# Kernel optimization log

Hardware: AMD Instinct MI355X
Metric: run time of the kernel (lower is better)

Reference implementation:

```python
import jax, jax.numpy as jnp
import numpy as np

LOCAL_RADIUS = 5


def setup_inputs() -> dict:
    key = jax.random.key(0)
    k1, k2, k3 = jax.random.split(key, 3)
    B, K, C, H = 4, 4096, 256, 128
    x = jax.random.normal(k1, (B, K, C), dtype=jnp.float32)
    W1 = jax.random.normal(k2, (C, H), dtype=jnp.float32) * (1.0 / np.sqrt(C))
    b1 = jnp.zeros((H,), dtype=jnp.float32)
    W2 = jax.random.normal(k3, (H, 1), dtype=jnp.float32) * (1.0 / np.sqrt(H))
    b2 = jnp.zeros((1,), dtype=jnp.float32)
    return {"x": x, "W1": W1, "b1": b1, "W2": W2, "b2": b2}


def reference(x, W1, b1, W2, b2):
    # x: [B, k, C]. The MLP score for column j is independent of the row i,
    # so compute it once per token instead of per (i, window) as in the torch loop.
    B, k, C = x.shape
    s = (jnp.tanh(x @ W1 + b1) @ W2 + b2)[..., 0]  # [B, k]
    idx = jnp.arange(k)
    band = (jnp.abs(idx[:, None] - idx[None, :]) <= LOCAL_RADIUS)  # [k, k]
    # Outside the band the original leaves scores at 0.0 (not -inf), so
    # out-of-window positions still contribute exp(0)=1 to the softmax.
    scores = jnp.where(band[None, :, :], s[:, None, :], jnp.float32(0.0))  # [B, k, k]
    weights = jax.nn.softmax(scores, axis=-1)  # [B, k, k]
    weighted = jnp.einsum('bij,bjc->bic', weights, x)  # [B, k, C]
    return weighted, weights
```

## Files before the change

kernel.cpp:

```cpp
#include <hip/hip_runtime.h>
#include <math.h>

#define B_ 4
#define K_ 4096
#define C_ 256
#define H_ 128
#define RAD 5
#define ROWS 8

typedef float floatx4 __attribute__((ext_vector_type(4)));


__global__ __launch_bounds__(128) void score_kernel(
    const float* __restrict__ x, const float* __restrict__ W1,
    const float* __restrict__ b1, const float* __restrict__ W2,
    const float* __restrict__ b2, float* __restrict__ s_out)
{
    const int tid = threadIdx.x;
    const int t0 = blockIdx.x * 8;
    const float* xr[8];
    #pragma unroll
    for (int t = 0; t < 8; ++t) xr[t] = x + (size_t)(t0 + t) * C_;

    float acc[8];
    float binit = b1[tid];
    #pragma unroll
    for (int t = 0; t < 8; ++t) acc[t] = binit;

    for (int c = 0; c < C_; c += 4) {
        float w0 = W1[(c + 0) * H_ + tid];
        float w1 = W1[(c + 1) * H_ + tid];
        float w2 = W1[(c + 2) * H_ + tid];
        float w3 = W1[(c + 3) * H_ + tid];
        #pragma unroll
        for (int t = 0; t < 8; ++t) {
            floatx4 xv = *(const floatx4*)&xr[t][c];
            acc[t] = fmaf(xv.x, w0, acc[t]);
            acc[t] = fmaf(xv.y, w1, acc[t]);
            acc[t] = fmaf(xv.z, w2, acc[t]);
            acc[t] = fmaf(xv.w, w3, acc[t]);
        }
    }

    __shared__ float red[2][8];
    float w2v = W2[tid];
    #pragma unroll
    for (int t = 0; t < 8; ++t) {
        float p = tanhf(acc[t]) * w2v;
        #pragma unroll
        for (int off = 32; off > 0; off >>= 1) p += __shfl_down(p, off);
        if ((tid & 63) == 0) red[tid >> 6][t] = p;
    }
    __syncthreads();
    if (tid < 8) s_out[t0 + tid] = red[0][tid] + red[1][tid] + b2[0];
}

__global__ __launch_bounds__(256) void colsum_partial(
    const float* __restrict__ x, float* __restrict__ partial)
{
    const int tid = threadIdx.x;
    const int blk = blockIdx.x;
    const float* base = x + (size_t)blk * 32 * C_ + tid;
    float a0 = 0.f, a1 = 0.f, a2 = 0.f, a3 = 0.f;
    #pragma unroll
    for (int kk = 0; kk < 32; kk += 4) {
        a0 += base[(size_t)(kk + 0) * C_];
        a1 += base[(size_t)(kk + 1) * C_];
        a2 += base[(size_t)(kk + 2) * C_];
        a3 += base[(size_t)(kk + 3) * C_];
    }
    partial[(size_t)blk * C_ + tid] = (a0 + a1) + (a2 + a3);
}

__global__ __launch_bounds__(256) void colsum_final(
    const float* __restrict__ partial, float* __restrict__ Ssum)
{
    const int tid = threadIdx.x;
    const int b = blockIdx.x;
    float acc = 0.f;
    for (int chunk = 0; chunk < 128; ++chunk)
        acc += partial[(size_t)(b * 128 + chunk) * C_ + tid];
    Ssum[b * C_ + tid] = acc;
}

__global__ __launch_bounds__(256) void attn_kernel(
    const float* __restrict__ x, const float* __restrict__ s,
    const float* __restrict__ Ssum, float* __restrict__ out)
{
    const int tid = threadIdx.x;
    const int blk = blockIdx.x;
    const int b  = blk >> 9;
    const int i0 = (blk & 511) * ROWS;

    const int j0t = max(0, i0 - RAD);
    const int j1t = min(K_ - 1, i0 + ROWS - 1 + RAD);
    const int ntok = j1t - j0t + 1;

    __shared__ float xs[ROWS + 2 * RAD][C_];
    __shared__ float sb[ROWS + 2 * RAD];
    __shared__ float wb[ROWS][2 * RAD + 1];
    __shared__ float woff[ROWS];

    if (tid < ntok) sb[tid] = s[b * K_ + j0t + tid];
    const floatx4* xsrc = (const floatx4*)(x + ((size_t)b * K_ + j0t) * C_);
    floatx4* xdst = (floatx4*)&xs[0][0];
    for (int f = tid; f < ntok * (C_ / 4); f += 256) xdst[f] = xsrc[f];
    __syncthreads();

    if (tid < ROWS) {
        const int i = i0 + tid;
        const int j0 = max(0, i - RAD), j1 = min(K_ - 1, i + RAD);
        const int nb = j1 - j0 + 1;
        float m = 0.f;
        for (int j = j0; j <= j1; ++j) m = fmaxf(m, sb[j - j0t]);
        float e0 = expf(-m);
        float D = (float)(K_ - nb) * e0;
        for (int j = j0; j <= j1; ++j) {
            float e = expf(sb[j - j0t] - m);
            wb[tid][j - j0] = e;
            D += e;
        }
        float inv = 1.0f / D;
        for (int jj = 0; jj < nb; ++jj) wb[tid][jj] *= inv;
        woff[tid] = e0 * inv;
    }
    __syncthreads();

    const float sc = Ssum[b * C_ + tid];

    #pragma unroll
    for (int r = 0; r < ROWS; ++r) {
        const int i = i0 + r;
        const int j0 = max(0, i - RAD), j1 = min(K_ - 1, i + RAD);
        const float wo = woff[r];
        floatx4* wrow4 = (floatx4*)(out + (size_t)B_ * K_ * C_ + ((size_t)b * K_ + i) * K_);
        #pragma unroll
        for (int q = 0; q < 4; ++q) {
            const int f = tid + 256 * q;
            const int jb = f * 4;
            floatx4 v = { wo, wo, wo, wo };
            if (jb + 3 >= j0 && jb <= j1) {
                if (jb + 0 >= j0 && jb + 0 <= j1) v.x = wb[r][jb + 0 - j0];
                if (jb + 1 >= j0 && jb + 1 <= j1) v.y = wb[r][jb + 1 - j0];
                if (jb + 2 >= j0 && jb + 2 <= j1) v.z = wb[r][jb + 2 - j0];
                if (jb + 3 >= j0 && jb + 3 <= j1) v.w = wb[r][jb + 3 - j0];
            }
            wrow4[f] = v;
        }
    }

    #pragma unroll
    for (int r = 0; r < ROWS; ++r) {
        const int i = i0 + r;
        const int j0 = max(0, i - RAD), j1 = min(K_ - 1, i + RAD);
        const float wo = woff[r];
        float acc = wo * sc;
        for (int j = j0; j <= j1; ++j)
            acc = fmaf(wb[r][j - j0] - wo, xs[j - j0t][tid], acc);
        out[((size_t)b * K_ + i) * C_ + tid] = acc;
    }
}

extern "C" void kernel_launch(void* const* d_in, const int* in_sizes, int n_in,
                              void* d_out, int out_size, void* d_ws, size_t ws_size,
                              hipStream_t stream) {
    const float* x  = (const float*)d_in[0];
    const float* W1 = (const float*)d_in[1];
    const float* b1 = (const float*)d_in[2];
    const float* W2 = (const float*)d_in[3];
    const float* b2 = (const float*)d_in[4];
    float* out = (float*)d_out;

    float* ws   = (float*)d_ws;
    float* s    = ws;
    float* Ssum = ws + B_ * K_;
    float* partial = out + (size_t)B_ * K_ * C_;

    score_kernel  <<<B_ * K_ / 8,    128, 0, stream>>>(x, W1, b1, W2, b2, s);
    colsum_partial<<<B_ * 128,       256, 0, stream>>>(x, partial);
    colsum_final  <<<B_,             256, 0, stream>>>(partial, Ssum);
    attn_kernel   <<<B_ * K_ / ROWS, 256, 0, stream>>>(x, s, Ssum, out);
}
```

Measured before the change: 379.8 us.

## Fuse score MLP and column-sum finalization into the attention kernel

Removes the separate score and colsum_final kernels. Each attention block now recomputes the MLP scores for its 18-token halo band and reduces the per-chunk column sums itself. It also drops the shared-memory x tile, reading x directly from global memory with float4 loads for the weighted output. This cuts two launches and the global round-trips for s and Ssum. In exchange it recomputes the MLP roughly 2.25x and makes every block re-read all 128 partial-sum chunks for its batch, which adds heavy L2 traffic.

Result: slower. 441.6 us (+16.3%).

```diff
diff --git a/kernel.cpp b/kernel.cpp
--- a/kernel.cpp
+++ b/kernel.cpp
@@ -7,53 +7,10 @@
 #define H_ 128
 #define RAD 5
 #define ROWS 8
+#define BAND (ROWS + 2 * RAD)
+#define NB   (2 * RAD + 1)
 
 typedef float floatx4 __attribute__((ext_vector_type(4)));
-
-
-__global__ __launch_bounds__(128) void score_kernel(
-    const float* __restrict__ x, const float* __restrict__ W1,
-    const float* __restrict__ b1, const float* __restrict__ W2,
-    const float* __restrict__ b2, float* __restrict__ s_out)
-{
-    const int tid = threadIdx.x;
-    const int t0 = blockIdx.x * 8;
-    const float* xr[8];
-    #pragma unroll
-    for (int t = 0; t < 8; ++t) xr[t] = x + (size_t)(t0 + t) * C_;
-
-    float acc[8];
-    float binit = b1[tid];
-    #pragma unroll
-    for (int t = 0; t < 8; ++t) acc[t] = binit;
-
-    for (int c = 0; c < C_; c += 4) {
-        float w0 = W1[(c + 0) * H_ + tid];
-        float w1 = W1[(c + 1) * H_ + tid];
-        float w2 = W1[(c + 2) * H_ + tid];
-        float w3 = W1[(c + 3) * H_ + tid];
-        #pragma unroll
-        for (int t = 0; t < 8; ++t) {
-            floatx4 xv = *(const floatx4*)&xr[t][c];
-            acc[t] = fmaf(xv.x, w0, acc[t]);
-            acc[t] = fmaf(xv.y, w1, acc[t]);
-            acc[t] = fmaf(xv.z, w2, acc[t]);
-            acc[t] = fmaf(xv.w, w3, acc[t]);
-        }
-    }
-
-    __shared__ float red[2][8];
-    float w2v = W2[tid];
-    #pragma unroll
-    for (int t = 0; t < 8; ++t) {
-        float p = tanhf(acc[t]) * w2v;
-        #pragma unroll
-        for (int off = 32; off > 0; off >>= 1) p += __shfl_down(p, off);
-        if ((tid & 63) == 0) red[tid >> 6][t] = p;
-    }
-    __syncthreads();
-    if (tid < 8) s_out[t0 + tid] = red[0][tid] + red[1][tid] + b2[0];
-}
 
 __global__ __launch_bounds__(256) void colsum_partial(
     const float* __restrict__ x, float* __restrict__ partial)
@@ -72,20 +29,11 @@
     partial[(size_t)blk * C_ + tid] = (a0 + a1) + (a2 + a3);
 }
 
-__global__ __launch_bounds__(256) void colsum_final(
-    const float* __restrict__ partial, float* __restrict__ Ssum)
-{
-    const int tid = threadIdx.x;
-    const int b = blockIdx.x;
-    float acc = 0.f;
-    for (int chunk = 0; chunk < 128; ++chunk)
-        acc += partial[(size_t)(b * 128 + chunk) * C_ + tid];
-    Ssum[b * C_ + tid] = acc;
-}
-
-__global__ __launch_bounds__(256) void attn_kernel(
-    const float* __restrict__ x, const float* __restrict__ s,
-    const float* __restrict__ Ssum, float* __restrict__ out)
+__global__ __launch_bounds__(256, 4) void fused_attn(
+    const float* __restrict__ x, const float* __restrict__ W1,
+    const float* __restrict__ b1, const float* __restrict__ W2,
+    const float* __restrict__ b2, const float* __restrict__ partial,
+    float* __restrict__ out)
 {
     const int tid = threadIdx.x;
     const int blk = blockIdx.x;
@@ -96,16 +44,64 @@
     const int j1t = min(K_ - 1, i0 + ROWS - 1 + RAD);
     const int ntok = j1t - j0t + 1;
 
-    __shared__ float xs[ROWS + 2 * RAD][C_];
-    __shared__ float sb[ROWS + 2 * RAD];
-    __shared__ float wb[ROWS][2 * RAD + 1];
+    __shared__ float red[4][9];
+    __shared__ float sb[BAND];
+    __shared__ float wb[ROWS][NB];
     __shared__ float woff[ROWS];
+    __shared__ float ssum[C_];
 
-    if (tid < ntok) sb[tid] = s[b * K_ + j0t + tid];
-    const floatx4* xsrc = (const floatx4*)(x + ((size_t)b * K_ + j0t) * C_);
-    floatx4* xdst = (floatx4*)&xs[0][0];
-    for (int f = tid; f < ntok * (C_ / 4); f += 256) xdst[f] = xsrc[f];
+    {
+        const int h = tid & 127;
+        const int g = tid >> 7;
+        const float* xbase = x + ((size_t)b * K_ + j0t) * C_;
+        const float* xp[9];
+        #pragma unroll
+        for (int t = 0; t < 9; ++t) {
+            int tt = g * 9 + t;
+            if (tt > ntok - 1) tt = ntok - 1;
+            xp[t] = xbase + (size_t)tt * C_;
+        }
+        float acc[9];
+        float binit = b1[h];
+        #pragma unroll
+        for (int t = 0; t < 9; ++t) acc[t] = binit;
+
+        for (int c = 0; c < C_; c += 4) {
+            float w0 = W1[(c + 0) * H_ + h];
+            float w1 = W1[(c + 1) * H_ + h];
+            float w2 = W1[(c + 2) * H_ + h];
+            float w3 = W1[(c + 3) * H_ + h];
+            #pragma unroll
+            for (int t = 0; t < 9; ++t) {
+                floatx4 xv = *(const floatx4*)(xp[t] + c);
+                acc[t] = fmaf(xv.x, w0, acc[t]);
+                acc[t] = fmaf(xv.y, w1, acc[t]);
+                acc[t] = fmaf(xv.z, w2, acc[t]);
+                acc[t] = fmaf(xv.w, w3, acc[t]);
+            }
+        }
+        float w2v = W2[h];
+        const int w = tid >> 6;
+        #pragma unroll
+        for (int t = 0; t < 9; ++t) {
+            float p = tanhf(acc[t]) * w2v;
+            #pragma unroll
+            for (int off = 32; off > 0; off >>= 1) p += __shfl_down(p, off);
+            if ((tid & 63) == 0) red[w][t] = p;
+        }
+    }
     __syncthreads();
+    if (tid < BAND) {
+        const int gg = tid / 9, t9 = tid % 9;
+        sb[tid] = red[2 * gg][t9] + red[2 * gg + 1][t9] + b2[0];
+    }
+    __syncthreads();
+
+    float ss = 0.f;
+    {
+        const float* pb = partial + (size_t)b * 128 * C_ + tid;
+        for (int ch = 0; ch < 128; ++ch) ss += pb[(size_t)ch * C_];
+    }
 
     if (tid < ROWS) {
         const int i = i0 + tid;
@@ -124,9 +120,31 @@
         for (int jj = 0; jj < nb; ++jj) wb[tid][jj] *= inv;
         woff[tid] = e0 * inv;
     }
+    ssum[tid] = ss;
     __syncthreads();
 
-    const float sc = Ssum[b * C_ + tid];
+    {
+        const int ct = tid & 63;
+        const floatx4 sc4 = ((const floatx4*)ssum)[ct];
+        #pragma unroll
+        for (int rr = 0; rr < 2; ++rr) {
+            const int r = (tid >> 6) + rr * 4;
+            const int i = i0 + r;
+            const int j0 = max(0, i - RAD), j1 = min(K_ - 1, i + RAD);
+            const float wo = woff[r];
+            floatx4 acc4 = { wo * sc4.x, wo * sc4.y, wo * sc4.z, wo * sc4.w };
+            const floatx4* xr = (const floatx4*)(x + ((size_t)b * K_) * C_) + ct;
+            for (int j = j0; j <= j1; ++j) {
+                const float wd = wb[r][j - j0] - wo;
+                floatx4 xv = xr[(size_t)j * (C_ / 4)];
+                acc4.x = fmaf(wd, xv.x, acc4.x);
+                acc4.y = fmaf(wd, xv.y, acc4.y);
+                acc4.z = fmaf(wd, xv.z, acc4.z);
+                acc4.w = fmaf(wd, xv.w, acc4.w);
+            }
+            ((floatx4*)(out + ((size_t)b * K_ + i) * C_))[ct] = acc4;
+        }
+    }
 
     #pragma unroll
     for (int r = 0; r < ROWS; ++r) {
@@ -148,17 +166,6 @@
             wrow4[f] = v;
         }
     }
-
-    #pragma unroll
-    for (int r = 0; r < ROWS; ++r) {
-        const int i = i0 + r;
-        const int j0 = max(0, i - RAD), j1 = min(K_ - 1, i + RAD);
-        const float wo = woff[r];
-        float acc = wo * sc;
-        for (int j = j0; j <= j1; ++j)
-            acc = fmaf(wb[r][j - j0] - wo, xs[j - j0t][tid], acc);
-        out[((size_t)b * K_ + i) * C_ + tid] = acc;
-    }
 }
 
 extern "C" void kernel_launch(void* const* d_in, const int* in_sizes, int n_in,
@@ -170,14 +177,8 @@
     const float* W2 = (const float*)d_in[3];
     const float* b2 = (const float*)d_in[4];
     float* out = (float*)d_out;
+    float* partial = (float*)d_ws;
 
-    float* ws   = (float*)d_ws;
-    float* s    = ws;
-    float* Ssum = ws + B_ * K_;
-    float* partial = out + (size_t)B_ * K_ * C_;
-
-    score_kernel  <<<B_ * K_ / 8,    128, 0, stream>>>(x, W1, b1, W2, b2, s);
     colsum_partial<<<B_ * 128,       256, 0, stream>>>(x, partial);
-    colsum_final  <<<B_,             256, 0, stream>>>(partial, Ssum);
-    attn_kernel   <<<B_ * K_ / ROWS, 256, 0, stream>>>(x, s, Ssum, out);
+    fused_attn    <<<B_ * K_ / ROWS, 256, 0, stream>>>(x, W1, b1, W2, b2, partial, out);
 }
```
